# Optimization experiments

Measured on AMD Instinct MI355X. Metric: run time of the kernel, lower is better.

## Reference

```python
import jax, jax.numpy as jnp
import numpy as np

B, S, D = 4, 2048, 1024
O = 1024
E = 8
K = 2

def setup_inputs() -> dict:
    key = jax.random.key(0)
    k1, k2, k3, k4, k5 = jax.random.split(key, 5)
    scale = 1.0 / np.sqrt(D)
    x = jax.random.normal(k1, (B, S, D), dtype=jnp.float32)
    # expert linear layers stacked: weight [E, D, O], bias [E, O]
    We = jax.random.uniform(k2, (E, D, O), dtype=jnp.float32, minval=-scale, maxval=scale)
    be = jax.random.uniform(k3, (E, O), dtype=jnp.float32, minval=-scale, maxval=scale)
    # gate linear: weight [D, E], bias [E]
    Wg = jax.random.uniform(k4, (D, E), dtype=jnp.float32, minval=-scale, maxval=scale)
    bg = jax.random.uniform(k5, (E,), dtype=jnp.float32, minval=-scale, maxval=scale)
    return {"x": x, "We": We, "be": be, "Wg": Wg, "bg": bg}

def reference(x, We, be, Wg, bg):
    b, s, d = x.shape
    x_flat = x.reshape(-1, d)                                   # [N, D]
    gates = jax.nn.softmax(x_flat @ Wg + bg, axis=-1)           # [N, E]
    topk_gates, topk_idx = jax.lax.top_k(gates, K)              # [N, K]
    topk_gates = topk_gates / jnp.sum(topk_gates, axis=1, keepdims=True)
    # dense all-expert compute (faithful to original naive MoE)
    expert_out = jnp.einsum('nd,edo->neo', x_flat, We) + be     # [N, E, O]
    # gather top-k expert outputs per token
    selected = jnp.take_along_axis(expert_out, topk_idx[:, :, None], axis=1)  # [N, K, O]
    out = jnp.sum(selected * topk_gates[:, :, None], axis=1)    # [N, O]
    return out.reshape(b, s, -1)
```

## Files before the change

### kernel.cpp

```cpp
#include <hip/hip_runtime.h>

#define N_TOK 8192
#define DDIM 1024
#define ODIM 1024
#define NEXP 8

typedef __attribute__((ext_vector_type(8))) short bf16x8;
typedef __attribute__((ext_vector_type(4))) float f32x4;

__device__ __forceinline__ unsigned int f2bf(float f) {
    unsigned int u = __float_as_uint(f);
    return (u + 0x7fffu + ((u >> 16) & 1u)) >> 16;
}
__device__ __forceinline__ float bflo(unsigned int u) { return __uint_as_float(u << 16); }
__device__ __forceinline__ float bfhi(unsigned int u) { return __uint_as_float(u & 0xffff0000u); }

__device__ __forceinline__ void async_copy16(const unsigned short* g, unsigned short* l) {
    __builtin_amdgcn_global_load_lds(
        (const __attribute__((address_space(1))) unsigned int*)g,
        (__attribute__((address_space(3))) unsigned int*)l, 16, 0, 0);
}

__global__ __launch_bounds__(256) void wet_kernel(const float* __restrict__ We,
                                                  unsigned short* __restrict__ WeT) {
    __shared__ float tile[64][65];
    const int e = blockIdx.z, d0 = blockIdx.x * 64, o0 = blockIdx.y * 64;
    const int tid = threadIdx.x;
#pragma unroll
    for (int p = 0; p < 4; ++p) {
        int idx = p * 256 + tid;
        int row = idx >> 4, c = idx & 15;
        float4 v = *(const float4*)&We[(((size_t)e * 1024 + d0 + row) << 10) + o0 + (c << 2)];
        tile[row][c * 4 + 0] = v.x; tile[row][c * 4 + 1] = v.y;
        tile[row][c * 4 + 2] = v.z; tile[row][c * 4 + 3] = v.w;
    }
    __syncthreads();
#pragma unroll
    for (int p = 0; p < 2; ++p) {
        int idx = p * 256 + tid;
        int orow = idx >> 3, c8 = idx & 7;
        unsigned int u[8];
#pragma unroll
        for (int j = 0; j < 8; ++j) u[j] = f2bf(tile[c8 * 8 + j][orow]);
        uint4 q;
        q.x = u[0] | (u[1] << 16); q.y = u[2] | (u[3] << 16);
        q.z = u[4] | (u[5] << 16); q.w = u[6] | (u[7] << 16);
        *(uint4*)&WeT[(((size_t)e * 1024 + o0 + orow) << 10) + d0 + (c8 << 3)] = q;
    }
}

__global__ __launch_bounds__(256) void gate_kernel(const float* __restrict__ x,
                                                   const float* __restrict__ Wg,
                                                   const float* __restrict__ bg,
                                                   int* __restrict__ ea, int* __restrict__ eb,
                                                   float* __restrict__ ga, float* __restrict__ gb,
                                                   unsigned short* __restrict__ xbf) {
    const int wave = threadIdx.x >> 6, lane = threadIdx.x & 63;
    const int t = blockIdx.x * 4 + wave;
    const float* xr = x + (size_t)t * DDIM;

    float4 v[4];
#pragma unroll
    for (int c = 0; c < 4; ++c) v[c] = *(const float4*)&xr[c * 256 + lane * 4];

    unsigned short* xo = xbf + (size_t)t * DDIM;
#pragma unroll
    for (int c = 0; c < 4; ++c) {
        uint2 w;
        w.x = f2bf(v[c].x) | (f2bf(v[c].y) << 16);
        w.y = f2bf(v[c].z) | (f2bf(v[c].w) << 16);
        *(uint2*)&xo[c * 256 + lane * 4] = w;
    }

    float acc[8] = {0, 0, 0, 0, 0, 0, 0, 0};
#pragma unroll
    for (int c = 0; c < 4; ++c) {
        const int dbase = c * 256 + lane * 4;
#pragma unroll
        for (int j = 0; j < 4; ++j) {
            float xv = ((const float*)&v[c])[j];
            const float4* w = (const float4*)(Wg + (size_t)(dbase + j) * 8);
            float4 w0 = w[0], w1 = w[1];
            acc[0] += xv * w0.x; acc[1] += xv * w0.y; acc[2] += xv * w0.z; acc[3] += xv * w0.w;
            acc[4] += xv * w1.x; acc[5] += xv * w1.y; acc[6] += xv * w1.z; acc[7] += xv * w1.w;
        }
    }
#pragma unroll
    for (int off = 32; off > 0; off >>= 1) {
#pragma unroll
        for (int j = 0; j < 8; ++j) acc[j] += __shfl_xor(acc[j], off, 64);
    }
    if (lane == 0) {
        float s[8];
#pragma unroll
        for (int e = 0; e < 8; ++e) s[e] = acc[e] + bg[e];
        int a = 0;
#pragma unroll
        for (int e = 1; e < 8; ++e) if (s[e] > s[a]) a = e;
        int b = (a == 0) ? 1 : 0;
#pragma unroll
        for (int e = 0; e < 8; ++e) if (e != a && e != b && s[e] > s[b]) b = e;
        float g0 = 1.0f / (1.0f + __expf(s[b] - s[a]));
        ea[t] = a; eb[t] = b; ga[t] = g0; gb[t] = 1.0f - g0;
    }
}

__global__ __launch_bounds__(256) void scatter_kernel(const int* __restrict__ ea,
                                                      const int* __restrict__ eb,
                                                      int* __restrict__ counts,
                                                      int* __restrict__ btok,
                                                      int* __restrict__ slotA,
                                                      int* __restrict__ slotB) {
    const int t = blockIdx.x * 256 + threadIdx.x;
    const int lane = threadIdx.x & 63;
#pragma unroll
    for (int pass = 0; pass < 2; ++pass) {
        const int e = (pass == 0) ? ea[t] : eb[t];
        int* slot = (pass == 0) ? slotA : slotB;
#pragma unroll
        for (int ex = 0; ex < NEXP; ++ex) {
            unsigned long long mask = __ballot(e == ex);
            if (mask) {
                int leader = __ffsll((long long)mask) - 1;
                int base = 0;
                if (lane == leader) base = atomicAdd(&counts[ex * 32], __popcll(mask));
                base = __shfl(base, leader, 64);
                if (e == ex) {
                    int pos = base + __popcll(mask & ((1ull << lane) - 1ull));
                    btok[ex * N_TOK + pos] = t;
                    slot[t] = ex * N_TOK + pos;
                }
            }
        }
    }
}

__global__ __launch_bounds__(256) void moe_gemm(const unsigned short* __restrict__ xbf,
                                                const unsigned short* __restrict__ WeT,
                                                const float* __restrict__ be,
                                                const int* __restrict__ counts,
                                                const int* __restrict__ btok,
                                                unsigned short* __restrict__ ybuf) {
    const int e = blockIdx.z;
    const int cnt = counts[e * 32];
    const int r0 = blockIdx.y * 128;
    if (r0 >= cnt) return;
    const int n0 = blockIdx.x * 128;

    __shared__ unsigned short sA[128 * 64];
    __shared__ unsigned short sB[128 * 64];
    __shared__ int s_tok[128];

    const int tid = threadIdx.x;
    if (tid < 128) {
        int r = r0 + tid;
        int rc = (r < cnt) ? r : (cnt - 1);
        s_tok[tid] = btok[e * N_TOK + rc];
    }
    const int wave = tid >> 6, lane = tid & 63;
    __syncthreads();

    const int colo = (((lane & 7) ^ (lane >> 3)) * 8);
    size_t a_off[4];
    size_t b_off[4];
#pragma unroll
    for (int p = 0; p < 4; ++p) {
        int row = wave * 32 + p * 8 + (lane >> 3);
        a_off[p] = ((size_t)s_tok[row] << 10) + colo;
        b_off[p] = (((size_t)e * 1024 + n0 + row) << 10) + colo;
    }

    const int wm = (wave >> 1) * 64, wn = (wave & 1) * 64;
    const int quad = lane >> 4, rA = lane & 15;
    const int sw = rA & 7;

    f32x4 acc[4][4];
#pragma unroll
    for (int mi = 0; mi < 4; ++mi)
#pragma unroll
        for (int ni = 0; ni < 4; ++ni) acc[mi][ni] = (f32x4){0.f, 0.f, 0.f, 0.f};

    for (int kb = 0; kb < DDIM; kb += 64) {
#pragma unroll
        for (int p = 0; p < 4; ++p) {
            unsigned short* la = &sA[(wave * 32 + p * 8) * 64];
            unsigned short* lb = &sB[(wave * 32 + p * 8) * 64];
            async_copy16(xbf + a_off[p] + kb, la);
            async_copy16(WeT + b_off[p] + kb, lb);
        }
        __syncthreads();
#pragma unroll
        for (int ks = 0; ks < 2; ++ks) {
            const int cslot = ((ks * 4 + quad) ^ sw) * 8;
            bf16x8 af[4], bfr[4];
#pragma unroll
            for (int mi = 0; mi < 4; ++mi)
                af[mi] = *(bf16x8*)&sA[(wm + mi * 16 + rA) * 64 + cslot];
#pragma unroll
            for (int ni = 0; ni < 4; ++ni)
                bfr[ni] = *(bf16x8*)&sB[(wn + ni * 16 + rA) * 64 + cslot];
#pragma unroll
            for (int mi = 0; mi < 4; ++mi)
#pragma unroll
                for (int ni = 0; ni < 4; ++ni)
                    acc[mi][ni] = __builtin_amdgcn_mfma_f32_16x16x32_bf16(af[mi], bfr[ni], acc[mi][ni], 0, 0, 0);
        }
        __syncthreads();
    }

#pragma unroll
    for (int ni = 0; ni < 4; ++ni) {
        int col = n0 + wn + ni * 16 + rA;
        float bias = be[(e << 10) + col];
#pragma unroll
        for (int mi = 0; mi < 4; ++mi) {
#pragma unroll
            for (int r = 0; r < 4; ++r) {
                int lrow = wm + mi * 16 + quad * 4 + r;
                if (r0 + lrow < cnt) {
                    ybuf[(((size_t)e * N_TOK + r0 + lrow) << 10) + col] =
                        (unsigned short)f2bf(acc[mi][ni][r] + bias);
                }
            }
        }
    }
}

__global__ __launch_bounds__(256) void combine_kernel(const unsigned short* __restrict__ ybuf,
                                                      const int* __restrict__ slotA,
                                                      const int* __restrict__ slotB,
                                                      const float* __restrict__ ga,
                                                      const float* __restrict__ gb,
                                                      float* __restrict__ out) {
    const int wave = threadIdx.x >> 6, lane = threadIdx.x & 63;
    const int t = blockIdx.x * 4 + wave;
    const unsigned short* ra = ybuf + ((size_t)slotA[t] << 10);
    const unsigned short* rb = ybuf + ((size_t)slotB[t] << 10);
    const float a = ga[t], b = gb[t];
    float* orow = out + ((size_t)t << 10);
#pragma unroll
    for (int i = 0; i < 4; ++i) {
        int c = i * 256 + lane * 4;
        uint2 ua = *(const uint2*)&ra[c];
        uint2 ub = *(const uint2*)&rb[c];
        float4 o;
        o.x = a * bflo(ua.x) + b * bflo(ub.x);
        o.y = a * bfhi(ua.x) + b * bfhi(ub.x);
        o.z = a * bflo(ua.y) + b * bflo(ub.y);
        o.w = a * bfhi(ua.y) + b * bfhi(ub.y);
        *(float4*)&orow[c] = o;
    }
}

extern "C" void kernel_launch(void* const* d_in, const int* in_sizes, int n_in,
                              void* d_out, int out_size, void* d_ws, size_t ws_size,
                              hipStream_t stream) {
    const float* x  = (const float*)d_in[0];
    const float* We = (const float*)d_in[1];
    const float* be = (const float*)d_in[2];
    const float* Wg = (const float*)d_in[3];
    const float* bg = (const float*)d_in[4];
    float* out = (float*)d_out;

    char* ws = (char*)d_ws;
    size_t off = 0;
    int* counts = (int*)(ws + off); off += 8 * 32 * 4;
    int* btok   = (int*)(ws + off); off += NEXP * N_TOK * 4;
    int* slotA  = (int*)(ws + off); off += N_TOK * 4;
    int* slotB  = (int*)(ws + off); off += N_TOK * 4;
    int* ea = (int*)(ws + off); off += N_TOK * 4;
    int* eb = (int*)(ws + off); off += N_TOK * 4;
    float* ga = (float*)(ws + off); off += N_TOK * 4;
    float* gb = (float*)(ws + off); off += N_TOK * 4;
    unsigned short* WeT  = (unsigned short*)(ws + off); off += (size_t)NEXP * DDIM * ODIM * 2;
    unsigned short* xbf  = (unsigned short*)(ws + off); off += (size_t)N_TOK * DDIM * 2;
    unsigned short* ybuf = (unsigned short*)(ws + off); off += (size_t)NEXP * N_TOK * ODIM * 2;

    hipMemsetAsync(counts, 0, 8 * 32 * sizeof(int), stream);

    wet_kernel<<<dim3(16, 16, 8), 256, 0, stream>>>(We, WeT);
    gate_kernel<<<dim3(N_TOK / 4), 256, 0, stream>>>(x, Wg, bg, ea, eb, ga, gb, xbf);
    scatter_kernel<<<dim3(N_TOK / 256), 256, 0, stream>>>(ea, eb, counts, btok, slotA, slotB);
    moe_gemm<<<dim3(ODIM / 128, N_TOK / 128, NEXP), 256, 0, stream>>>(xbf, WeT, be, counts, btok, ybuf);
    combine_kernel<<<dim3(N_TOK / 4), 256, 0, stream>>>(ybuf, slotA, slotB, ga, gb, out);
}
```

Before: 246.6 us.

## Load MFMA operands directly from global memory, drop LDS staging and memset

```diff
diff --git a/kernel.cpp b/kernel.cpp
--- a/kernel.cpp
+++ b/kernel.cpp
@@ -14,12 +14,6 @@
 }
 __device__ __forceinline__ float bflo(unsigned int u) { return __uint_as_float(u << 16); }
 __device__ __forceinline__ float bfhi(unsigned int u) { return __uint_as_float(u & 0xffff0000u); }
-
-__device__ __forceinline__ void async_copy16(const unsigned short* g, unsigned short* l) {
-    __builtin_amdgcn_global_load_lds(
-        (const __attribute__((address_space(1))) unsigned int*)g,
-        (__attribute__((address_space(3))) unsigned int*)l, 16, 0, 0);
-}
 
 __global__ __launch_bounds__(256) void wet_kernel(const float* __restrict__ We,
                                                   unsigned short* __restrict__ WeT) {
@@ -54,7 +48,9 @@
                                                    const float* __restrict__ bg,
                                                    int* __restrict__ ea, int* __restrict__ eb,
                                                    float* __restrict__ ga, float* __restrict__ gb,
-                                                   unsigned short* __restrict__ xbf) {
+                                                   unsigned short* __restrict__ xbf,
+                                                   int* __restrict__ counts) {
+    if (blockIdx.x == 0) counts[threadIdx.x] = 0;
     const int wave = threadIdx.x >> 6, lane = threadIdx.x & 63;
     const int t = blockIdx.x * 4 + wave;
     const float* xr = x + (size_t)t * DDIM;
@@ -105,13 +101,13 @@
     }
 }
 
-__global__ __launch_bounds__(256) void scatter_kernel(const int* __restrict__ ea,
-                                                      const int* __restrict__ eb,
-                                                      int* __restrict__ counts,
-                                                      int* __restrict__ btok,
-                                                      int* __restrict__ slotA,
-                                                      int* __restrict__ slotB) {
-    const int t = blockIdx.x * 256 + threadIdx.x;
+__global__ __launch_bounds__(64) void scatter_kernel(const int* __restrict__ ea,
+                                                     const int* __restrict__ eb,
+                                                     int* __restrict__ counts,
+                                                     int* __restrict__ btok,
+                                                     int* __restrict__ slotA,
+                                                     int* __restrict__ slotB) {
+    const int t = blockIdx.x * 64 + threadIdx.x;
     const int lane = threadIdx.x & 63;
 #pragma unroll
     for (int pass = 0; pass < 2; ++pass) {
@@ -147,32 +143,27 @@
     if (r0 >= cnt) return;
     const int n0 = blockIdx.x * 128;
 
-    __shared__ unsigned short sA[128 * 64];
-    __shared__ unsigned short sB[128 * 64];
     __shared__ int s_tok[128];
-
     const int tid = threadIdx.x;
     if (tid < 128) {
         int r = r0 + tid;
         int rc = (r < cnt) ? r : (cnt - 1);
         s_tok[tid] = btok[e * N_TOK + rc];
     }
+    __syncthreads();
+
     const int wave = tid >> 6, lane = tid & 63;
-    __syncthreads();
-
-    const int colo = (((lane & 7) ^ (lane >> 3)) * 8);
-    size_t a_off[4];
-    size_t b_off[4];
-#pragma unroll
-    for (int p = 0; p < 4; ++p) {
-        int row = wave * 32 + p * 8 + (lane >> 3);
-        a_off[p] = ((size_t)s_tok[row] << 10) + colo;
-        b_off[p] = (((size_t)e * 1024 + n0 + row) << 10) + colo;
-    }
-
     const int wm = (wave >> 1) * 64, wn = (wave & 1) * 64;
     const int quad = lane >> 4, rA = lane & 15;
-    const int sw = rA & 7;
+
+    const unsigned short* aptr[4];
+    const unsigned short* bptr[4];
+#pragma unroll
+    for (int mi = 0; mi < 4; ++mi)
+        aptr[mi] = xbf + ((size_t)s_tok[wm + mi * 16 + rA] << 10) + quad * 8;
+#pragma unroll
+    for (int ni = 0; ni < 4; ++ni)
+        bptr[ni] = WeT + (((size_t)e * 1024 + n0 + wn + ni * 16 + rA) << 10) + quad * 8;
 
     f32x4 acc[4][4];
 #pragma unroll
@@ -180,32 +171,21 @@
 #pragma unroll
         for (int ni = 0; ni < 4; ++ni) acc[mi][ni] = (f32x4){0.f, 0.f, 0.f, 0.f};
 
-    for (int kb = 0; kb < DDIM; kb += 64) {
-#pragma unroll
-        for (int p = 0; p < 4; ++p) {
-            unsigned short* la = &sA[(wave * 32 + p * 8) * 64];
-            unsigned short* lb = &sB[(wave * 32 + p * 8) * 64];
-            async_copy16(xbf + a_off[p] + kb, la);
-            async_copy16(WeT + b_off[p] + kb, lb);
-        }
-        __syncthreads();
-#pragma unroll
-        for (int ks = 0; ks < 2; ++ks) {
-            const int cslot = ((ks * 4 + quad) ^ sw) * 8;
+    for (int kb = 0; kb < DDIM; kb += 256) {
+#pragma unroll
+        for (int ks = 0; ks < 8; ++ks) {
+            const int ko = kb + ks * 32;
             bf16x8 af[4], bfr[4];
 #pragma unroll
-            for (int mi = 0; mi < 4; ++mi)
-                af[mi] = *(bf16x8*)&sA[(wm + mi * 16 + rA) * 64 + cslot];
-#pragma unroll
-            for (int ni = 0; ni < 4; ++ni)
-                bfr[ni] = *(bf16x8*)&sB[(wn + ni * 16 + rA) * 64 + cslot];
+            for (int mi = 0; mi < 4; ++mi) af[mi] = *(const bf16x8*)(aptr[mi] + ko);
+#pragma unroll
+            for (int ni = 0; ni < 4; ++ni) bfr[ni] = *(const bf16x8*)(bptr[ni] + ko);
 #pragma unroll
             for (int mi = 0; mi < 4; ++mi)
 #pragma unroll
                 for (int ni = 0; ni < 4; ++ni)
                     acc[mi][ni] = __builtin_amdgcn_mfma_f32_16x16x32_bf16(af[mi], bfr[ni], acc[mi][ni], 0, 0, 0);
         }
-        __syncthreads();
     }
 
 #pragma unroll
@@ -276,11 +256,9 @@
     unsigned short* xbf  = (unsigned short*)(ws + off); off += (size_t)N_TOK * DDIM * 2;
     unsigned short* ybuf = (unsigned short*)(ws + off); off += (size_t)NEXP * N_TOK * ODIM * 2;
 
-    hipMemsetAsync(counts, 0, 8 * 32 * sizeof(int), stream);
-
     wet_kernel<<<dim3(16, 16, 8), 256, 0, stream>>>(We, WeT);
-    gate_kernel<<<dim3(N_TOK / 4), 256, 0, stream>>>(x, Wg, bg, ea, eb, ga, gb, xbf);
-    scatter_kernel<<<dim3(N_TOK / 256), 256, 0, stream>>>(ea, eb, counts, btok, slotA, slotB);
+    gate_kernel<<<dim3(N_TOK / 4), 256, 0, stream>>>(x, Wg, bg, ea, eb, ga, gb, xbf, counts);
+    scatter_kernel<<<dim3(N_TOK / 64), 64, 0, stream>>>(ea, eb, counts, btok, slotA, slotB);
     moe_gemm<<<dim3(ODIM / 128, N_TOK / 128, NEXP), 256, 0, stream>>>(xbf, WeT, be, counts, btok, ybuf);
     combine_kernel<<<dim3(N_TOK / 4), 256, 0, stream>>>(ybuf, slotA, slotB, ga, gb, out);
 }
```

Result: slower. 349.5 us (+41.8%).
